# Performance work log

Measured on AMD Instinct MI355X. Metric: run time of the kernel, lower is better.

The kernel has to match this reference:

```python
import jax, jax.numpy as jnp
import numpy as np

N, B, OBS, ACT, E = 8, 8192, 128, 32, 128  # num_agents, batch, obs, act, embedding_dim


def setup_inputs() -> dict:
    key = jax.random.key(0)
    ks = jax.random.split(key, 14)
    rn = lambda k, shape: jax.random.normal(k, shape, dtype=jnp.float32) * 0.05
    return {
        'obs': jax.random.normal(ks[0], (N, B, OBS), dtype=jnp.float32),
        'act': jax.random.normal(ks[1], (N, B, ACT), dtype=jnp.float32),
        'Wg': rn(ks[2], (N, OBS + ACT, E)), 'bg': rn(ks[3], (N, E)),
        'Wq': rn(ks[4], (N, E, E)), 'bq': rn(ks[5], (N, E)),
        'Wk': rn(ks[6], (N, E, E)), 'bk': rn(ks[7], (N, E)),
        'Wv': rn(ks[8], (N, E, E)), 'bv': rn(ks[9], (N, E)),
        'W1': rn(ks[10], (N, (N + 1) * E, E)), 'b1': rn(ks[11], (N, E)),
        'W2': rn(ks[12], (N, E, 1)), 'b2': rn(ks[13], (N, 1)),
    }


def reference(obs, act, Wg, bg, Wq, bq, Wk, bk, Wv, bv, W1, b1, W2, b2):
    # per-agent embeddings e_i = relu(g_i([obs_i; act_i]))           [N,B,E]
    oa = jnp.concatenate([obs, act], axis=-1)
    e = jax.nn.relu(jnp.einsum('nbd,nde->nbe', oa, Wg) + bg[:, None, :])

    # per-(agent i, head l) queries and per-(agent j, head l) keys   [N,L,B,E]
    q = jnp.einsum('ibe,lef->ilbf', e, Wq) + bq[None, :, None, :]
    k = jnp.einsum('jbe,lef->jlbf', e, Wk) + bk[None, :, None, :]

    # scalar per-sample score key.dot(query); original applies softmax to this
    # single scalar, which is identically 1 -> softmax over a singleton axis.
    scores = jnp.einsum('ilbe,jlbe->iljb', q, k)          # [N,L,N,B]
    alpha = jax.nn.softmax(scores[..., None], axis=-1)[..., 0]  # == ones

    # values v_{l,j} = leaky_relu(V_l(e_j))                          [L,N,B,E]
    v = jax.nn.leaky_relu(jnp.einsum('jbe,lef->ljbf', e, Wv) + bv[:, None, None, :])

    # exclude j == i, aggregate: total_{i,l} = sum_{j!=i} alpha * v_{l,j}
    mask = (1.0 - jnp.eye(N, dtype=e.dtype))              # [i,j]
    w = alpha * mask[:, None, :, None]                    # [N,L,N,B]
    total = jnp.einsum('iljb,ljbe->ilbe', w, v)           # [N,L,B,E]

    # x_i = concat over heads l -> [N,B,L*E]
    xi = jnp.transpose(total, (0, 2, 1, 3)).reshape(N, B, N * E)

    # q_i = f_i([x_i; e_i])
    h = jnp.concatenate([xi, e], axis=-1)                 # [N,B,(N+1)E]
    h = jax.nn.relu(jnp.einsum('nbd,nde->nbe', h, W1) + b1[:, None, :])
    out = jnp.einsum('nbe,neo->nbo', h, W2) + b2[:, None, :]  # [N,B,1]
    return out
```

## Files before the change

### kernel.cpp

```cpp
#include <hip/hip_runtime.h>

#define DEV static __device__ __forceinline__

typedef __attribute__((ext_vector_type(8))) short short8;
typedef __attribute__((ext_vector_type(8))) __bf16 bf16x8;
typedef __attribute__((ext_vector_type(4))) float f32x4;


DEV short f2bf(float f) { return __builtin_bit_cast(short, (__bf16)f); }
DEV float bf2f(short h) {
  unsigned u = ((unsigned)(unsigned short)h) << 16;
  return __builtin_bit_cast(float, u);
}
DEV f32x4 mfma16(short8 a, short8 b, f32x4 c) {
  return __builtin_amdgcn_mfma_f32_16x16x32_bf16(
      __builtin_bit_cast(bf16x8, a), __builtin_bit_cast(bf16x8, b), c, 0, 0, 0);
}
DEV void async_copy16(short* lds, const short* g) {
  __builtin_amdgcn_global_load_lds(
      (const __attribute__((address_space(1))) void*)g,
      (__attribute__((address_space(3))) void*)lds, 16, 0, 0);
}

template <int GPC, int SRC_STRIDE, int LDS_STRIDE>
DEV void stage_bt(short* lds, const short* src, int tid) {
  constexpr int TOTAL = 128 * GPC;
  #pragma unroll
  for (int g0 = 0; g0 < TOTAL; g0 += 256) {
    int g = g0 + tid;
    int c = g / GPC, kg = g % GPC;
    *(short8*)(lds + c * LDS_STRIDE + kg * 8) =
        *(const short8*)(src + c * SRC_STRIDE + kg * 8);
  }
}

__global__ __launch_bounds__(256) void k0_tr(const float* __restrict__ Wg,
                                             const float* __restrict__ Wv,
                                             const float* __restrict__ W1,
                                             short* __restrict__ WgT,
                                             short* __restrict__ WvP,
                                             short* __restrict__ W1P) {
  int g = blockIdx.x * 256 + threadIdx.x;
  short8 o;
  if (g < 20480) {
    int n = g / 2560, rem = g % 2560;
    int c = rem & 127, kg = rem >> 7;
    const float* src = Wg + n * 20480;
    #pragma unroll
    for (int j = 0; j < 8; ++j) o[j] = f2bf(src[(size_t)(kg * 8 + j) * 128 + c]);
    *(short8*)(WgT + n * 20480 + c * 160 + kg * 8) = o;
  } else if (g < 36864) {
    int g2 = g - 20480;
    int n = g2 >> 11, rem = g2 & 2047;
    int c = rem & 127, kg = rem >> 7;
    const float* src = Wv + n * 16384;
    #pragma unroll
    for (int j = 0; j < 8; ++j) o[j] = f2bf(src[(size_t)(16 * j + kg) * 128 + c]);
    *(short8*)(WvP + n * 16384 + c * 128 + kg * 8) = o;
  } else {
    int g3 = g - 36864;
    int n = g3 / 18432, rem = g3 % 18432;
    int c = rem & 127, kg = rem >> 7;
    int chunk = kg >> 4, kl = kg & 15;
    const float* src = W1 + (size_t)n * 147456;
    #pragma unroll
    for (int j = 0; j < 8; ++j)
      o[j] = f2bf(src[(size_t)(chunk * 128 + 16 * j + kl) * 128 + c]);
    *(short8*)(W1P + (size_t)n * 147456 + c * 1152 + kg * 8) = o;
  }
}

__global__ __launch_bounds__(256) void k1_e(const float* __restrict__ obs,
                                            const float* __restrict__ act,
                                            const short* __restrict__ WgT,
                                            const float* __restrict__ bg,
                                            short* __restrict__ eB) {
  __shared__ __align__(16) short BW[128 * 168];
  const int btile = blockIdx.x, n = blockIdx.y, tid = threadIdx.x;
  stage_bt<20, 160, 168>(BW, WgT + n * 20480, tid);
  __syncthreads();
  const int lane = tid & 63, wave = tid >> 6, lr = lane & 15, kg = lane >> 4;
  const int rowbase = btile * 64 + wave * 16;
  f32x4 acc[8];
  #pragma unroll
  for (int m = 0; m < 8; ++m) acc[m] = f32x4{0.f, 0.f, 0.f, 0.f};
  const float* obsp = obs + (size_t)(n * 8192 + rowbase + lr) * 128;
  const float* actp = act + (size_t)(n * 8192 + rowbase + lr) * 32;
  #pragma unroll
  for (int ks = 0; ks < 5; ++ks) {
    const float* ap = (ks < 4) ? (obsp + ks * 32 + kg * 8) : (actp + kg * 8);
    float4 p0 = *(const float4*)ap;
    float4 p1 = *(const float4*)(ap + 4);
    short8 a;
    a[0] = f2bf(p0.x); a[1] = f2bf(p0.y); a[2] = f2bf(p0.z); a[3] = f2bf(p0.w);
    a[4] = f2bf(p1.x); a[5] = f2bf(p1.y); a[6] = f2bf(p1.z); a[7] = f2bf(p1.w);
    #pragma unroll
    for (int m = 0; m < 8; ++m) {
      short8 b = *(const short8*)(&BW[(m * 16 + lr) * 168 + ks * 32 + kg * 8]);
      acc[m] = mfma16(a, b, acc[m]);
    }
  }
  float bgv[8];
  #pragma unroll
  for (int m = 0; m < 8; ++m) bgv[m] = bg[n * 128 + m * 16 + lr];
  #pragma unroll
  for (int r = 0; r < 4; ++r) {
    short8 pkt;
    #pragma unroll
    for (int m = 0; m < 8; ++m) {
      float x = acc[m][r] + bgv[m];
      pkt[m] = f2bf(x > 0.f ? x : 0.f);
    }
    *(short8*)(eB + (size_t)(n * 8192 + rowbase + kg * 4 + r) * 128 + lr * 8) = pkt;
  }
}

__global__ __launch_bounds__(256) void k2_S(const short* __restrict__ eB,
                                            const short* __restrict__ WvP,
                                            const float* __restrict__ bv,
                                            short* __restrict__ SB) {
  __shared__ __align__(16) short BW[128 * 136];
  const int btile = blockIdx.x, l = blockIdx.y, tid = threadIdx.x;
  stage_bt<16, 128, 136>(BW, WvP + l * 16384, tid);
  __syncthreads();
  const int lane = tid & 63, wave = tid >> 6, lr = lane & 15, kg = lane >> 4;
  const int rowbase = btile * 64 + wave * 16;
  f32x4 Sacc[8];
  #pragma unroll
  for (int m = 0; m < 8; ++m) Sacc[m] = f32x4{0.f, 0.f, 0.f, 0.f};
  float bvv[8];
  #pragma unroll
  for (int m = 0; m < 8; ++m) bvv[m] = bv[l * 128 + m * 16 + lr];
  for (int j = 0; j < 8; ++j) {
    f32x4 acc[8];
    #pragma unroll
    for (int m = 0; m < 8; ++m) acc[m] = f32x4{0.f, 0.f, 0.f, 0.f};
    const short* ep = eB + (size_t)(j * 8192 + rowbase + lr) * 128;
    #pragma unroll
    for (int ks = 0; ks < 4; ++ks) {
      short8 a = *(const short8*)(ep + ks * 32 + kg * 8);
      #pragma unroll
      for (int m = 0; m < 8; ++m) {
        short8 b = *(const short8*)(&BW[(m * 16 + lr) * 136 + ks * 32 + kg * 8]);
        acc[m] = mfma16(a, b, acc[m]);
      }
    }
    #pragma unroll
    for (int m = 0; m < 8; ++m)
      #pragma unroll
      for (int r = 0; r < 4; ++r) {
        float x = acc[m][r] + bvv[m];
        Sacc[m][r] += (x > 0.f ? x : 0.01f * x);
      }
  }
  #pragma unroll
  for (int r = 0; r < 4; ++r) {
    short8 pkt;
    #pragma unroll
    for (int m = 0; m < 8; ++m) pkt[m] = f2bf(Sacc[m][r]);
    *(short8*)(SB + (size_t)(l * 8192 + rowbase + kg * 4 + r) * 128 + lr * 8) = pkt;
  }
}

__global__ __launch_bounds__(512, 2) void k3_f(const short* __restrict__ eB,
                                               const short* __restrict__ SB,
                                               const short* __restrict__ WvP,
                                               const short* __restrict__ W1P,
                                               const float* __restrict__ bv,
                                               const float* __restrict__ b1,
                                               const float* __restrict__ W2,
                                               const float* __restrict__ b2,
                                               float* __restrict__ out) {
  __shared__ __align__(16) short BW[2][128 * 128];
  __shared__ __align__(16) short VB[8][8 * 128];
  const int bid = blockIdx.x;
  const int i = bid & 7;
  const int btile = bid >> 3;
  const int tid = threadIdx.x;
  const int lane = tid & 63, wave = tid >> 6, lr = lane & 15, kg = lane >> 4;
  const int lr8 = lane & 7;
  const int rowbase = btile * 256 + wave * 32;
  const short* w1 = W1P + (size_t)i * 147456;
  short* vb = VB[wave];

#define STAGE_WV(buf, l)                                                       \
  {                                                                            \
    _Pragma("unroll") for (int t = 0; t < 4; ++t) {                            \
      int G = t * 512 + tid;                                                   \
      int cG = G >> 4, gl = G & 15;                                            \
      async_copy16((buf) + (t * 512 + wave * 64) * 8,                          \
                   WvP + (l) * 16384 + cG * 128 + ((gl ^ (cG & 7)) << 3));     \
    }                                                                          \
  }
#define STAGE_W1(buf, koff)                                                    \
  {                                                                            \
    _Pragma("unroll") for (int t = 0; t < 4; ++t) {                            \
      int G = t * 512 + tid;                                                   \
      int cG = G >> 4, gl = G & 15;                                            \
      async_copy16((buf) + (t * 512 + wave * 64) * 8,                          \
                   w1 + cG * 1152 + (koff) + ((gl ^ (cG & 7)) << 3));          \
    }                                                                          \
  }

  short8 ea[2][4];
  #pragma unroll
  for (int s = 0; s < 2; ++s)
    #pragma unroll
    for (int ks = 0; ks < 4; ++ks)
      ea[s][ks] = *(const short8*)(
          eB + (size_t)(i * 8192 + rowbase + s * 16 + lr) * 128 + (ks * 4 + kg) * 8);

  f32x4 hacc[2][8];
  #pragma unroll
  for (int s = 0; s < 2; ++s)
    #pragma unroll
    for (int m = 0; m < 8; ++m) hacc[s][m] = f32x4{0.f, 0.f, 0.f, 0.f};
  short8 aa[2][4];

  STAGE_WV(BW[0], 0);
  for (int c = 0; c < 17; ++c) {
    __syncthreads();
    if (c < 16) {
      int nc = c + 1;
      if (nc == 16) { STAGE_W1(BW[0], 1024); }
      else if (nc & 1) { STAGE_W1(BW[1], (nc >> 1) * 128); }
      else { STAGE_WV(BW[0], nc >> 1); }
    }
    const short* bw = BW[c & 1];
    if (c == 16) {
      #pragma unroll
      for (int ks = 0; ks < 4; ++ks)
        #pragma unroll
        for (int m = 0; m < 8; ++m) {
          short8 b = *(const short8*)(bw + (m * 16 + lr) * 128 +
                                      (((ks * 4 + kg) ^ lr8) << 3));
          hacc[0][m] = mfma16(ea[0][ks], b, hacc[0][m]);
          hacc[1][m] = mfma16(ea[1][ks], b, hacc[1][m]);
        }
    } else if (c & 1) {
      #pragma unroll
      for (int ks = 0; ks < 4; ++ks)
        #pragma unroll
        for (int m = 0; m < 8; ++m) {
          short8 b = *(const short8*)(bw + (m * 16 + lr) * 128 +
                                      (((ks * 4 + kg) ^ lr8) << 3));
          hacc[0][m] = mfma16(aa[0][ks], b, hacc[0][m]);
          hacc[1][m] = mfma16(aa[1][ks], b, hacc[1][m]);
        }
    } else {
      const int l = c >> 1;
      float bvv[8];
      #pragma unroll
      for (int m = 0; m < 8; ++m) bvv[m] = bv[l * 128 + m * 16 + lr];
      #pragma unroll
      for (int s = 0; s < 2; ++s) {
        short8 sv[4];
        #pragma unroll
        for (int r = 0; r < 4; ++r)
          sv[r] = *(const short8*)(
              SB + (size_t)(l * 8192 + rowbase + s * 16 + kg * 4 + r) * 128 + lr * 8);
        f32x4 vacc[8];
        #pragma unroll
        for (int m = 0; m < 8; ++m) vacc[m] = f32x4{0.f, 0.f, 0.f, 0.f};
        #pragma unroll
        for (int ks = 0; ks < 4; ++ks)
          #pragma unroll
          for (int m = 0; m < 8; ++m) {
            short8 b = *(const short8*)(bw + (m * 16 + lr) * 128 +
                                        (((ks * 4 + kg) ^ lr8) << 3));
            vacc[m] = mfma16(ea[s][ks], b, vacc[m]);
          }
        short8 pkt[4];
        #pragma unroll
        for (int r = 0; r < 4; ++r)
          #pragma unroll
          for (int m = 0; m < 8; ++m) {
            float x = vacc[m][r] + bvv[m];
            x = (x > 0.f) ? x : 0.01f * x;
            pkt[r][m] = f2bf(bf2f(sv[r][m]) - x);
          }
        #pragma unroll
        for (int p = 0; p < 2; ++p) {
          if ((kg >> 1) == p) {
            #pragma unroll
            for (int r = 0; r < 4; ++r) {
              int rl = (kg & 1) * 4 + r;
              *(short8*)(vb + rl * 128 + ((lr ^ rl) << 3)) = pkt[r];
            }
          }
          if ((lr >> 3) == p) {
            int rl = lr & 7;
            #pragma unroll
            for (int ks = 0; ks < 4; ++ks)
              aa[s][ks] = *(const short8*)(vb + rl * 128 +
                                           (((ks * 4 + kg) ^ rl) << 3));
          }
        }
      }
    }
  }
#undef STAGE_WV
#undef STAGE_W1

  #pragma unroll
  for (int s = 0; s < 2; ++s) {
    float sacc[4] = {0.f, 0.f, 0.f, 0.f};
    #pragma unroll
    for (int m = 0; m < 8; ++m) {
      int col = m * 16 + lr;
      float b1v = b1[i * 128 + col];
      float w2v = W2[i * 128 + col];
      #pragma unroll
      for (int r = 0; r < 4; ++r) {
        float h = hacc[s][m][r] + b1v;
        h = h > 0.f ? h : 0.f;
        sacc[r] += h * w2v;
      }
    }
    #pragma unroll
    for (int r = 0; r < 4; ++r) {
      float v = sacc[r];
      v += __shfl_xor(v, 1);
      v += __shfl_xor(v, 2);
      v += __shfl_xor(v, 4);
      v += __shfl_xor(v, 8);
      if (lr == 0)
        out[i * 8192 + rowbase + s * 16 + kg * 4 + r] = v + b2[i];
    }
  }
}

extern "C" void kernel_launch(void* const* d_in, const int* in_sizes, int n_in,
                              void* d_out, int out_size, void* d_ws, size_t ws_size,
                              hipStream_t stream) {
  const float* obs = (const float*)d_in[0];
  const float* act = (const float*)d_in[1];
  const float* Wg  = (const float*)d_in[2];
  const float* bg  = (const float*)d_in[3];
  const float* Wv  = (const float*)d_in[8];
  const float* bv  = (const float*)d_in[9];
  const float* W1  = (const float*)d_in[10];
  const float* b1  = (const float*)d_in[11];
  const float* W2  = (const float*)d_in[12];
  const float* b2  = (const float*)d_in[13];
  float* out = (float*)d_out;

  short* eB  = (short*)d_ws;
  short* SB  = eB + (size_t)8 * 8192 * 128;
  short* WgT = SB + (size_t)8 * 8192 * 128;
  short* WvP = WgT + 163840;
  short* W1P = WvP + 131072;

  k0_tr<<<720, 256, 0, stream>>>(Wg, Wv, W1, WgT, WvP, W1P);
  k1_e<<<dim3(128, 8), 256, 0, stream>>>(obs, act, WgT, bg, eB);
  k2_S<<<dim3(128, 8), 256, 0, stream>>>(eB, WvP, bv, SB);
  k3_f<<<256, 512, 0, stream>>>(eB, SB, WvP, W1P, bv, b1, W2, b2, out);
}
```

Baseline: 111.7 us.

## Prefetch per-head S tiles into LDS and share Wv fragments across subtiles

The value-projection phase now stages each block's 256-row slice of SB for the current head into a new 64KB shared buffer. The load is asynchronous and issued together with the Wv staging, replacing direct per-thread global loads that sat on the critical path. The Wv GEMM for both 16-row subtiles is also computed in one loop, so each B fragment read from LDS feeds two MFMAs. In exchange, shared memory per block grows from about 80KB to about 144KB, which likely prevents two blocks from sharing a CU despite the launch bounds. The doubled vacc accumulators also add register pressure.

```diff
diff --git a/kernel.cpp b/kernel.cpp
--- a/kernel.cpp
+++ b/kernel.cpp
@@ -172,6 +172,7 @@
                                                const float* __restrict__ b2,
                                                float* __restrict__ out) {
   __shared__ __align__(16) short BW[2][128 * 128];
+  __shared__ __align__(16) short SBuf[256 * 128];
   __shared__ __align__(16) short VB[8][8 * 128];
   const int bid = blockIdx.x;
   const int i = bid & 7;
@@ -201,6 +202,16 @@
                    w1 + cG * 1152 + (koff) + ((gl ^ (cG & 7)) << 3));          \
     }                                                                          \
   }
+#define STAGE_SB(l)                                                            \
+  {                                                                            \
+    _Pragma("unroll") for (int t = 0; t < 8; ++t) {                            \
+      int G = t * 512 + tid;                                                   \
+      int row = G >> 4, gl = G & 15;                                           \
+      async_copy16(SBuf + (t * 512 + wave * 64) * 8,                           \
+                   SB + ((size_t)(l) * 8192 + btile * 256 + row) * 128 +       \
+                       gl * 8);                                                \
+    }                                                                          \
+  }
 
   short8 ea[2][4];
   #pragma unroll
@@ -218,13 +229,14 @@
   short8 aa[2][4];
 
   STAGE_WV(BW[0], 0);
+  STAGE_SB(0);
   for (int c = 0; c < 17; ++c) {
     __syncthreads();
     if (c < 16) {
       int nc = c + 1;
       if (nc == 16) { STAGE_W1(BW[0], 1024); }
       else if (nc & 1) { STAGE_W1(BW[1], (nc >> 1) * 128); }
-      else { STAGE_WV(BW[0], nc >> 1); }
+      else { STAGE_WV(BW[0], nc >> 1); STAGE_SB(nc >> 1); }
     }
     const short* bw = BW[c & 1];
     if (c == 16) {
@@ -252,33 +264,34 @@
       float bvv[8];
       #pragma unroll
       for (int m = 0; m < 8; ++m) bvv[m] = bv[l * 128 + m * 16 + lr];
+      f32x4 vacc[2][8];
+      #pragma unroll
+      for (int s = 0; s < 2; ++s)
+        #pragma unroll
+        for (int m = 0; m < 8; ++m) vacc[s][m] = f32x4{0.f, 0.f, 0.f, 0.f};
+      #pragma unroll
+      for (int ks = 0; ks < 4; ++ks)
+        #pragma unroll
+        for (int m = 0; m < 8; ++m) {
+          short8 b = *(const short8*)(bw + (m * 16 + lr) * 128 +
+                                      (((ks * 4 + kg) ^ lr8) << 3));
+          vacc[0][m] = mfma16(ea[0][ks], b, vacc[0][m]);
+          vacc[1][m] = mfma16(ea[1][ks], b, vacc[1][m]);
+        }
       #pragma unroll
       for (int s = 0; s < 2; ++s) {
-        short8 sv[4];
-        #pragma unroll
-        for (int r = 0; r < 4; ++r)
-          sv[r] = *(const short8*)(
-              SB + (size_t)(l * 8192 + rowbase + s * 16 + kg * 4 + r) * 128 + lr * 8);
-        f32x4 vacc[8];
-        #pragma unroll
-        for (int m = 0; m < 8; ++m) vacc[m] = f32x4{0.f, 0.f, 0.f, 0.f};
-        #pragma unroll
-        for (int ks = 0; ks < 4; ++ks)
+        short8 pkt[4];
+        #pragma unroll
+        for (int r = 0; r < 4; ++r) {
+          short8 sv = *(const short8*)(
+              SBuf + (wave * 32 + s * 16 + kg * 4 + r) * 128 + lr * 8);
           #pragma unroll
           for (int m = 0; m < 8; ++m) {
-            short8 b = *(const short8*)(bw + (m * 16 + lr) * 128 +
-                                        (((ks * 4 + kg) ^ lr8) << 3));
-            vacc[m] = mfma16(ea[s][ks], b, vacc[m]);
+            float x = vacc[s][m][r] + bvv[m];
+            x = (x > 0.f) ? x : 0.01f * x;
+            pkt[r][m] = f2bf(bf2f(sv[m]) - x);
           }
-        short8 pkt[4];
-        #pragma unroll
-        for (int r = 0; r < 4; ++r)
-          #pragma unroll
-          for (int m = 0; m < 8; ++m) {
-            float x = vacc[m][r] + bvv[m];
-            x = (x > 0.f) ? x : 0.01f * x;
-            pkt[r][m] = f2bf(bf2f(sv[r][m]) - x);
-          }
+        }
         #pragma unroll
         for (int p = 0; p < 2; ++p) {
           if ((kg >> 1) == p) {
@@ -301,6 +314,7 @@
   }
 #undef STAGE_WV
 #undef STAGE_W1
+#undef STAGE_SB
 
   #pragma unroll
   for (int s = 0; s < 2; ++s) {
```

After: 127.8 us. 14.4% more time.

## Materialize per-agent aggregated values in k2 and simplify k3 to a pure GEMM

Applied to the files above, without the earlier changes.

k2 now runs the V-projection twice. The first pass sums over all agents, and the second pass writes S minus v_j for every agent j and head l into a full [N,B,N*E] bf16 buffer. k3 no longer recomputes the value projection, stages only W1, and shrinks to a plain double-buffered GEMM with register prefetch of the next A chunk. This removes the recompute and LDS shuffle from k3. The cost is an intermediate about eight times larger, written and then read back through global memory, plus doubled GEMM work in k2.

```diff
diff --git a/kernel.cpp b/kernel.cpp
--- a/kernel.cpp
+++ b/kernel.cpp
@@ -115,22 +115,22 @@
   }
 }
 
-__global__ __launch_bounds__(256) void k2_S(const short* __restrict__ eB,
+__global__ __launch_bounds__(256) void k2_A(const short* __restrict__ eB,
                                             const short* __restrict__ WvP,
                                             const float* __restrict__ bv,
-                                            short* __restrict__ SB) {
+                                            short* __restrict__ AB) {
   __shared__ __align__(16) short BW[128 * 136];
   const int btile = blockIdx.x, l = blockIdx.y, tid = threadIdx.x;
   stage_bt<16, 128, 136>(BW, WvP + l * 16384, tid);
   __syncthreads();
   const int lane = tid & 63, wave = tid >> 6, lr = lane & 15, kg = lane >> 4;
   const int rowbase = btile * 64 + wave * 16;
+  float bvv[8];
+  #pragma unroll
+  for (int m = 0; m < 8; ++m) bvv[m] = bv[l * 128 + m * 16 + lr];
   f32x4 Sacc[8];
   #pragma unroll
   for (int m = 0; m < 8; ++m) Sacc[m] = f32x4{0.f, 0.f, 0.f, 0.f};
-  float bvv[8];
-  #pragma unroll
-  for (int m = 0; m < 8; ++m) bvv[m] = bv[l * 128 + m * 16 + lr];
   for (int j = 0; j < 8; ++j) {
     f32x4 acc[8];
     #pragma unroll
@@ -153,45 +153,52 @@
         Sacc[m][r] += (x > 0.f ? x : 0.01f * x);
       }
   }
-  #pragma unroll
-  for (int r = 0; r < 4; ++r) {
-    short8 pkt;
-    #pragma unroll
-    for (int m = 0; m < 8; ++m) pkt[m] = f2bf(Sacc[m][r]);
-    *(short8*)(SB + (size_t)(l * 8192 + rowbase + kg * 4 + r) * 128 + lr * 8) = pkt;
-  }
-}
-
-__global__ __launch_bounds__(512, 2) void k3_f(const short* __restrict__ eB,
-                                               const short* __restrict__ SB,
-                                               const short* __restrict__ WvP,
+  for (int j = 0; j < 8; ++j) {
+    f32x4 acc[8];
+    #pragma unroll
+    for (int m = 0; m < 8; ++m) acc[m] = f32x4{0.f, 0.f, 0.f, 0.f};
+    const short* ep = eB + (size_t)(j * 8192 + rowbase + lr) * 128;
+    #pragma unroll
+    for (int ks = 0; ks < 4; ++ks) {
+      short8 a = *(const short8*)(ep + ks * 32 + kg * 8);
+      #pragma unroll
+      for (int m = 0; m < 8; ++m) {
+        short8 b = *(const short8*)(&BW[(m * 16 + lr) * 136 + ks * 32 + kg * 8]);
+        acc[m] = mfma16(a, b, acc[m]);
+      }
+    }
+    #pragma unroll
+    for (int r = 0; r < 4; ++r) {
+      short8 pkt;
+      #pragma unroll
+      for (int m = 0; m < 8; ++m) {
+        float x = acc[m][r] + bvv[m];
+        x = (x > 0.f) ? x : 0.01f * x;
+        pkt[m] = f2bf(Sacc[m][r] - x);
+      }
+      *(short8*)(AB + (size_t)(j * 8192 + rowbase + kg * 4 + r) * 1024 +
+                 l * 128 + lr * 8) = pkt;
+    }
+  }
+}
+
+__global__ __launch_bounds__(512, 2) void k3_g(const short* __restrict__ eB,
+                                               const short* __restrict__ AB,
                                                const short* __restrict__ W1P,
-                                               const float* __restrict__ bv,
                                                const float* __restrict__ b1,
                                                const float* __restrict__ W2,
                                                const float* __restrict__ b2,
                                                float* __restrict__ out) {
   __shared__ __align__(16) short BW[2][128 * 128];
-  __shared__ __align__(16) short VB[8][8 * 128];
   const int bid = blockIdx.x;
   const int i = bid & 7;
   const int btile = bid >> 3;
   const int tid = threadIdx.x;
   const int lane = tid & 63, wave = tid >> 6, lr = lane & 15, kg = lane >> 4;
   const int lr8 = lane & 7;
-  const int rowbase = btile * 256 + wave * 32;
+  const int rowbase = btile * 128 + wave * 16;
   const short* w1 = W1P + (size_t)i * 147456;
-  short* vb = VB[wave];
-
-#define STAGE_WV(buf, l)                                                       \
-  {                                                                            \
-    _Pragma("unroll") for (int t = 0; t < 4; ++t) {                            \
-      int G = t * 512 + tid;                                                   \
-      int cG = G >> 4, gl = G & 15;                                            \
-      async_copy16((buf) + (t * 512 + wave * 64) * 8,                          \
-                   WvP + (l) * 16384 + cG * 128 + ((gl ^ (cG & 7)) << 3));     \
-    }                                                                          \
-  }
+
 #define STAGE_W1(buf, koff)                                                    \
   {                                                                            \
     _Pragma("unroll") for (int t = 0; t < 4; ++t) {                            \
@@ -202,131 +209,68 @@
     }                                                                          \
   }
 
-  short8 ea[2][4];
-  #pragma unroll
-  for (int s = 0; s < 2; ++s)
+  const short* abase = AB + (size_t)(i * 8192 + rowbase + lr) * 1024;
+  const short* ebase = eB + (size_t)(i * 8192 + rowbase + lr) * 128;
+
+  short8 ea[4], aa[4], aap[4];
+  #pragma unroll
+  for (int ks = 0; ks < 4; ++ks) {
+    ea[ks] = *(const short8*)(ebase + (ks * 4 + kg) * 8);
+    aa[ks] = *(const short8*)(abase + (ks * 4 + kg) * 8);
+  }
+  f32x4 hacc[8];
+  #pragma unroll
+  for (int m = 0; m < 8; ++m) hacc[m] = f32x4{0.f, 0.f, 0.f, 0.f};
+
+  STAGE_W1(BW[0], 0);
+  for (int c = 0; c < 9; ++c) {
+    __syncthreads();
+    if (c < 8) { STAGE_W1(BW[(c + 1) & 1], (c + 1 == 8) ? 1024 : (c + 1) * 128); }
+    if (c + 1 < 8) {
+      #pragma unroll
+      for (int ks = 0; ks < 4; ++ks)
+        aap[ks] = *(const short8*)(abase + (c + 1) * 128 + (ks * 4 + kg) * 8);
+    }
+    const short* bw = BW[c & 1];
     #pragma unroll
     for (int ks = 0; ks < 4; ++ks)
-      ea[s][ks] = *(const short8*)(
-          eB + (size_t)(i * 8192 + rowbase + s * 16 + lr) * 128 + (ks * 4 + kg) * 8);
-
-  f32x4 hacc[2][8];
-  #pragma unroll
-  for (int s = 0; s < 2; ++s)
-    #pragma unroll
-    for (int m = 0; m < 8; ++m) hacc[s][m] = f32x4{0.f, 0.f, 0.f, 0.f};
-  short8 aa[2][4];
-
-  STAGE_WV(BW[0], 0);
-  for (int c = 0; c < 17; ++c) {
-    __syncthreads();
-    if (c < 16) {
-      int nc = c + 1;
-      if (nc == 16) { STAGE_W1(BW[0], 1024); }
-      else if (nc & 1) { STAGE_W1(BW[1], (nc >> 1) * 128); }
-      else { STAGE_WV(BW[0], nc >> 1); }
-    }
-    const short* bw = BW[c & 1];
-    if (c == 16) {
-      #pragma unroll
-      for (int ks = 0; ks < 4; ++ks)
-        #pragma unroll
-        for (int m = 0; m < 8; ++m) {
-          short8 b = *(const short8*)(bw + (m * 16 + lr) * 128 +
-                                      (((ks * 4 + kg) ^ lr8) << 3));
-          hacc[0][m] = mfma16(ea[0][ks], b, hacc[0][m]);
-          hacc[1][m] = mfma16(ea[1][ks], b, hacc[1][m]);
-        }
-    } else if (c & 1) {
-      #pragma unroll
-      for (int ks = 0; ks < 4; ++ks)
-        #pragma unroll
-        for (int m = 0; m < 8; ++m) {
-          short8 b = *(const short8*)(bw + (m * 16 + lr) * 128 +
-                                      (((ks * 4 + kg) ^ lr8) << 3));
-          hacc[0][m] = mfma16(aa[0][ks], b, hacc[0][m]);
-          hacc[1][m] = mfma16(aa[1][ks], b, hacc[1][m]);
-        }
+      #pragma unroll
+      for (int m = 0; m < 8; ++m) {
+        short8 b = *(const short8*)(bw + (m * 16 + lr) * 128 +
+                                    (((ks * 4 + kg) ^ lr8) << 3));
+        hacc[m] = mfma16(aa[ks], b, hacc[m]);
+      }
+    if (c + 1 < 8) {
+      #pragma unroll
+      for (int ks = 0; ks < 4; ++ks) aa[ks] = aap[ks];
     } else {
-      const int l = c >> 1;
-      float bvv[8];
-      #pragma unroll
-      for (int m = 0; m < 8; ++m) bvv[m] = bv[l * 128 + m * 16 + lr];
-      #pragma unroll
-      for (int s = 0; s < 2; ++s) {
-        short8 sv[4];
-        #pragma unroll
-        for (int r = 0; r < 4; ++r)
-          sv[r] = *(const short8*)(
-              SB + (size_t)(l * 8192 + rowbase + s * 16 + kg * 4 + r) * 128 + lr * 8);
-        f32x4 vacc[8];
-        #pragma unroll
-        for (int m = 0; m < 8; ++m) vacc[m] = f32x4{0.f, 0.f, 0.f, 0.f};
-        #pragma unroll
-        for (int ks = 0; ks < 4; ++ks)
-          #pragma unroll
-          for (int m = 0; m < 8; ++m) {
-            short8 b = *(const short8*)(bw + (m * 16 + lr) * 128 +
-                                        (((ks * 4 + kg) ^ lr8) << 3));
-            vacc[m] = mfma16(ea[s][ks], b, vacc[m]);
-          }
-        short8 pkt[4];
-        #pragma unroll
-        for (int r = 0; r < 4; ++r)
-          #pragma unroll
-          for (int m = 0; m < 8; ++m) {
-            float x = vacc[m][r] + bvv[m];
-            x = (x > 0.f) ? x : 0.01f * x;
-            pkt[r][m] = f2bf(bf2f(sv[r][m]) - x);
-          }
-        #pragma unroll
-        for (int p = 0; p < 2; ++p) {
-          if ((kg >> 1) == p) {
-            #pragma unroll
-            for (int r = 0; r < 4; ++r) {
-              int rl = (kg & 1) * 4 + r;
-              *(short8*)(vb + rl * 128 + ((lr ^ rl) << 3)) = pkt[r];
-            }
-          }
-          if ((lr >> 3) == p) {
-            int rl = lr & 7;
-            #pragma unroll
-            for (int ks = 0; ks < 4; ++ks)
-              aa[s][ks] = *(const short8*)(vb + rl * 128 +
-                                           (((ks * 4 + kg) ^ rl) << 3));
-          }
-        }
-      }
-    }
-  }
-#undef STAGE_WV
+      #pragma unroll
+      for (int ks = 0; ks < 4; ++ks) aa[ks] = ea[ks];
+    }
+  }
 #undef STAGE_W1
 
-  #pragma unroll
-  for (int s = 0; s < 2; ++s) {
-    float sacc[4] = {0.f, 0.f, 0.f, 0.f};
-    #pragma unroll
-    for (int m = 0; m < 8; ++m) {
-      int col = m * 16 + lr;
-      float b1v = b1[i * 128 + col];
-      float w2v = W2[i * 128 + col];
-      #pragma unroll
-      for (int r = 0; r < 4; ++r) {
-        float h = hacc[s][m][r] + b1v;
-        h = h > 0.f ? h : 0.f;
-        sacc[r] += h * w2v;
-      }
-    }
+  float sacc[4] = {0.f, 0.f, 0.f, 0.f};
+  #pragma unroll
+  for (int m = 0; m < 8; ++m) {
+    int col = m * 16 + lr;
+    float b1v = b1[i * 128 + col];
+    float w2v = W2[i * 128 + col];
     #pragma unroll
     for (int r = 0; r < 4; ++r) {
-      float v = sacc[r];
-      v += __shfl_xor(v, 1);
-      v += __shfl_xor(v, 2);
-      v += __shfl_xor(v, 4);
-      v += __shfl_xor(v, 8);
-      if (lr == 0)
-        out[i * 8192 + rowbase + s * 16 + kg * 4 + r] = v + b2[i];
-    }
+      float h = hacc[m][r] + b1v;
+      h = h > 0.f ? h : 0.f;
+      sacc[r] += h * w2v;
+    }
+  }
+  #pragma unroll
+  for (int r = 0; r < 4; ++r) {
+    float v = sacc[r];
+    v += __shfl_xor(v, 1);
+    v += __shfl_xor(v, 2);
+    v += __shfl_xor(v, 4);
+    v += __shfl_xor(v, 8);
+    if (lr == 0) out[i * 8192 + rowbase + kg * 4 + r] = v + b2[i];
   }
 }
 
@@ -346,13 +290,13 @@
   float* out = (float*)d_out;
 
   short* eB  = (short*)d_ws;
-  short* SB  = eB + (size_t)8 * 8192 * 128;
-  short* WgT = SB + (size_t)8 * 8192 * 128;
+  short* AB  = eB + (size_t)8 * 8192 * 128;
+  short* WgT = AB + (size_t)8 * 8192 * 1024;
   short* WvP = WgT + 163840;
   short* W1P = WvP + 131072;
 
   k0_tr<<<720, 256, 0, stream>>>(Wg, Wv, W1, WgT, WvP, W1P);
   k1_e<<<dim3(128, 8), 256, 0, stream>>>(obs, act, WgT, bg, eB);
-  k2_S<<<dim3(128, 8), 256, 0, stream>>>(eB, WvP, bv, SB);
-  k3_f<<<256, 512, 0, stream>>>(eB, SB, WvP, W1P, bv, b1, W2, b2, out);
-}
+  k2_A<<<dim3(128, 8), 256, 0, stream>>>(eB, WvP, bv, AB);
+  k3_g<<<512, 512, 0, stream>>>(eB, AB, W1P, b1, W2, b2, out);
+}
```

Result: no change. 112.0 us (+0.3%).
